# Optimization experiments

Measured on AMD Instinct MI355X. Metric: run time of the kernel, lower is better.

Reference implementation:

```python
import jax, jax.numpy as jnp
import numpy as np

NUM_CODES = 512
DIM = 64
B, M = 32, 64


def setup_inputs() -> dict:
    key = jax.random.key(0)
    k1, k2 = jax.random.split(key)
    inputs = jax.random.normal(k1, (B, M, M, DIM), dtype=jnp.float32)
    # keras 'uniform' initializer is U(-0.05, 0.05)
    embeddings = jax.random.uniform(k2, (NUM_CODES, DIM), dtype=jnp.float32,
                                    minval=-0.05, maxval=0.05)
    return {"inputs": inputs, "embeddings": embeddings}


def reference(inputs, embeddings):
    l2_inputs = jnp.sum(inputs * inputs, axis=-1, keepdims=True)      # [B,M,M,1]
    l2_embeddings = jnp.sum(embeddings * embeddings, axis=-1)          # [K]
    dot = jnp.einsum('bhwd,kd->bhwk', inputs, embeddings)              # [B,M,M,K]
    distance = l2_inputs + l2_embeddings - 2.0 * dot                   # [B,M,M,K]
    codes = jnp.argmin(distance, axis=-1).astype(jnp.int32)            # [B,M,M]
    code_vecs = embeddings[codes]                                      # [B,M,M,D]
    return codes, code_vecs
```

## Files before the change

kernel.cpp:

```cpp
#include <hip/hip_runtime.h>

#define NUM_CODES 512
#define DIM 64
#define NPIX (32 * 64 * 64)
#define CT (NUM_CODES / 16)
#define BLK 256
#define NGRP 4
#define PPB 256

typedef __attribute__((ext_vector_type(8))) short bf16x8;
typedef __attribute__((ext_vector_type(4))) float f32x4;

__device__ __forceinline__ unsigned short f2bf(float f) {
    unsigned u = __float_as_uint(f);
    return (unsigned short)((u + 0x7fffu + ((u >> 16) & 1u)) >> 16);
}
__device__ __forceinline__ float bf2f(unsigned short h) {
    return __uint_as_float(((unsigned)h) << 16);
}

__global__ __launch_bounds__(256) void prep_kernel(
    const float* __restrict__ emb, unsigned short* __restrict__ AH,
    unsigned short* __restrict__ ALO, float* __restrict__ l2e,
    float* __restrict__ l2eh) {
    const int t = blockIdx.x * 256 + threadIdx.x;
    const int e0 = t * 4;
    const int c = e0 >> 6, d0 = e0 & 63;
    const float4 v = *(const float4*)(emb + c * DIM + d0);
    float f[4] = {v.x, v.y, v.z, v.w};
    unsigned short h[4], l[4];
#pragma unroll
    for (int i = 0; i < 4; ++i) {
        h[i] = f2bf(f[i]);
        l[i] = f2bf(f[i] - bf2f(h[i]));
    }
    const int ct = c >> 4, mr = c & 15, s = d0 >> 5, q = (d0 & 31) >> 3,
              j0 = d0 & 7;
    const int base = ((ct * 2 + s) * 64 + (q * 16 + mr)) * 8 + j0;
    *(ushort4*)(AH + base) = make_ushort4(h[0], h[1], h[2], h[3]);
    *(ushort4*)(ALO + base) = make_ushort4(l[0], l[1], l[2], l[3]);

    if (t < NUM_CODES) {
        const float* e = emb + t * DIM;
        float r[8];
#pragma unroll
        for (int j = 0; j < 8; ++j) {
            float w = e[j];
            r[j] = w * w;
        }
#pragma unroll
        for (int i = 8; i < DIM; i += 8)
#pragma unroll
            for (int j = 0; j < 8; ++j) {
                float w = e[i + j];
                r[j] += w * w;
            }
        float sv =
            ((r[0] + r[1]) + (r[2] + r[3])) + ((r[4] + r[5]) + (r[6] + r[7]));
        l2e[t] = sv;
        l2eh[t] = 0.5f * sv;
    }
}

__global__ __launch_bounds__(BLK, 2) void vq_main(
    const float* __restrict__ x_in, const unsigned short* __restrict__ AH,
    const unsigned short* __restrict__ ALO, const float* __restrict__ l2e,
    const float* __restrict__ l2eh, const float* __restrict__ emb,
    float* __restrict__ codes_out, float* __restrict__ vecs_out) {
    __shared__ float s_l2eh[NUM_CODES];
    __shared__ float s_l2ex[NUM_CODES];
    __shared__ int s_top[PPB][2];
    __shared__ int s_code[PPB];

    const int tid = threadIdx.x, lane = tid & 63, wave = tid >> 6;
    s_l2eh[tid] = l2eh[tid];
    s_l2eh[tid + 256] = l2eh[tid + 256];
    s_l2ex[tid] = l2e[tid];
    s_l2ex[tid + 256] = l2e[tid + 256];
    __syncthreads();

    const int p = lane & 15, q = lane >> 4;
    const int pw = blockIdx.x * PPB + wave * (16 * NGRP);

    bf16x8 bh0[NGRP], bl0[NGRP], bh1[NGRP], bl1[NGRP];
#pragma unroll
    for (int g = 0; g < NGRP; ++g) {
        const float* xb = x_in + (size_t)(pw + g * 16 + p) * DIM + q * 8;
        float4 u0 = *(const float4*)(xb);
        float4 u1 = *(const float4*)(xb + 4);
        float4 u2 = *(const float4*)(xb + 32);
        float4 u3 = *(const float4*)(xb + 36);
        float f0[8] = {u0.x, u0.y, u0.z, u0.w, u1.x, u1.y, u1.z, u1.w};
        float f1[8] = {u2.x, u2.y, u2.z, u2.w, u3.x, u3.y, u3.z, u3.w};
#pragma unroll
        for (int j = 0; j < 8; ++j) {
            unsigned short hh = f2bf(f0[j]);
            bh0[g][j] = (short)hh;
            bl0[g][j] = (short)f2bf(f0[j] - bf2f(hh));
            unsigned short h2 = f2bf(f1[j]);
            bh1[g][j] = (short)h2;
            bl1[g][j] = (short)f2bf(f1[j] - bf2f(h2));
        }
    }

    const int rowbase = q * 4;
    float d1[NGRP], d2[NGRP];
    int k1[NGRP], k2[NGRP];
#pragma unroll
    for (int g = 0; g < NGRP; ++g) {
        d1[g] = 3.4e38f;
        d2[g] = 3.4e38f;
        k1[g] = 0;
        k2[g] = 0;
    }

    const unsigned short* pAH = AH + lane * 8;
    const unsigned short* pAL = ALO + lane * 8;
    for (int ct = 0; ct < CT; ++ct) {
        const bf16x8 a0h = *(const bf16x8*)(pAH + ct * 1024);
        const bf16x8 a0l = *(const bf16x8*)(pAL + ct * 1024);
        const bf16x8 a1h = *(const bf16x8*)(pAH + ct * 1024 + 512);
        const bf16x8 a1l = *(const bf16x8*)(pAL + ct * 1024 + 512);
        const int kb = ct * 16 + rowbase;
        float l2v[4];
#pragma unroll
        for (int r = 0; r < 4; ++r) l2v[r] = s_l2eh[kb + r];

#pragma unroll
        for (int g = 0; g < NGRP; ++g) {
            f32x4 acc = {0.f, 0.f, 0.f, 0.f};
            acc = __builtin_amdgcn_mfma_f32_16x16x32_bf16(a0h, bh0[g], acc, 0, 0, 0);
            acc = __builtin_amdgcn_mfma_f32_16x16x32_bf16(a1h, bh1[g], acc, 0, 0, 0);
            acc = __builtin_amdgcn_mfma_f32_16x16x32_bf16(a0l, bh0[g], acc, 0, 0, 0);
            acc = __builtin_amdgcn_mfma_f32_16x16x32_bf16(a1l, bh1[g], acc, 0, 0, 0);
            acc = __builtin_amdgcn_mfma_f32_16x16x32_bf16(a0h, bl0[g], acc, 0, 0, 0);
            acc = __builtin_amdgcn_mfma_f32_16x16x32_bf16(a1h, bl1[g], acc, 0, 0, 0);

#pragma unroll
            for (int r = 0; r < 4; ++r) {
                const float d = l2v[r] - acc[r];
                const int kk = kb + r;
                const bool c = d < d1[g], c2 = d < d2[g];
                const float nd2 = c2 ? d : d2[g];
                const int nk2 = c2 ? kk : k2[g];
                d2[g] = c ? d1[g] : nd2;
                k2[g] = c ? k1[g] : nk2;
                k1[g] = c ? kk : k1[g];
                d1[g] = c ? d : d1[g];
            }
        }
    }

#pragma unroll
    for (int g = 0; g < NGRP; ++g) {
        float a1 = d1[g], a2 = d2[g];
        int b1 = k1[g], b2 = k2[g];
#pragma unroll
        for (int off = 16; off <= 32; off <<= 1) {
            const float od1 = __shfl_xor(a1, off);
            const int ok1 = __shfl_xor(b1, off);
            const float od2 = __shfl_xor(a2, off);
            const int ok2 = __shfl_xor(b2, off);
            const bool c = od1 < a1;
            const float w1 = c ? od1 : a1;
            const int wk1 = c ? ok1 : b1;
            const float l1 = c ? a1 : od1;
            const int lk1 = c ? b1 : ok1;
            const bool cm = od2 < a2;
            const float m2 = cm ? od2 : a2;
            const int mk2 = cm ? ok2 : b2;
            const bool c3 = m2 < l1;
            a2 = c3 ? m2 : l1;
            b2 = c3 ? mk2 : lk1;
            a1 = w1;
            b1 = wk1;
        }
        if (lane < 16) {
            s_top[wave * (16 * NGRP) + g * 16 + lane][0] = b1;
            s_top[wave * (16 * NGRP) + g * 16 + lane][1] = b2;
        }
    }
    __syncthreads();

    {
        const int pix = blockIdx.x * PPB + tid;
        int ka = s_top[tid][0], kb2 = s_top[tid][1];
        if (kb2 < ka) {
            const int tt = ka;
            ka = kb2;
            kb2 = tt;
        }
        const float* xr = x_in + (size_t)pix * DIM;
        float x[DIM];
#pragma unroll
        for (int jj = 0; jj < 16; ++jj) {
            const float4 v = *(const float4*)(xr + jj * 4);
            x[4 * jj + 0] = v.x;
            x[4 * jj + 1] = v.y;
            x[4 * jj + 2] = v.z;
            x[4 * jj + 3] = v.w;
        }
        float r[8];
#pragma unroll
        for (int j = 0; j < 8; ++j) r[j] = x[j] * x[j];
#pragma unroll
        for (int i = 8; i < DIM; i += 8)
#pragma unroll
            for (int j = 0; j < 8; ++j) r[j] += x[i + j] * x[i + j];
        const float l2x =
            ((r[0] + r[1]) + (r[2] + r[3])) + ((r[4] + r[5]) + (r[6] + r[7]));

        const float* ea = emb + (size_t)ka * DIM;
        float acca = 0.f;
#pragma unroll
        for (int d = 0; d < DIM; ++d) acca = __builtin_fmaf(x[d], ea[d], acca);
        const float da = (l2x + s_l2ex[ka]) - 2.0f * acca;

        const float* eb = emb + (size_t)kb2 * DIM;
        float accb = 0.f;
#pragma unroll
        for (int d = 0; d < DIM; ++d) accb = __builtin_fmaf(x[d], eb[d], accb);
        const float db = (l2x + s_l2ex[kb2]) - 2.0f * accb;

        const int sel = (db < da) ? kb2 : ka;
        s_code[tid] = sel;
        codes_out[pix] = (float)sel;
    }
    __syncthreads();

    const float4* emb4 = (const float4*)emb;
    float4* vout4 = (float4*)(vecs_out + (size_t)blockIdx.x * PPB * DIM);
#pragma unroll
    for (int it = 0; it < (PPB * DIM / 4) / BLK; ++it) {
        const int fidx = tid + it * BLK;
        const int pp = fidx >> 4, dd = fidx & 15;
        vout4[fidx] = emb4[(size_t)s_code[pp] * (DIM / 4) + dd];
    }
}

extern "C" void kernel_launch(void* const* d_in, const int* in_sizes, int n_in,
                              void* d_out, int out_size, void* d_ws,
                              size_t ws_size, hipStream_t stream) {
    const float* x_in = (const float*)d_in[0];
    const float* emb = (const float*)d_in[1];

    unsigned short* AH = (unsigned short*)d_ws;
    unsigned short* ALO = AH + NUM_CODES * DIM;
    float* l2e = (float*)(ALO + NUM_CODES * DIM);
    float* l2eh = l2e + NUM_CODES;

    float* codes_out = (float*)d_out;
    float* vecs_out = (float*)d_out + NPIX;

    hipLaunchKernelGGL(prep_kernel, dim3(32), dim3(256), 0, stream, emb, AH,
                       ALO, l2e, l2eh);
    hipLaunchKernelGGL(vq_main, dim3(NPIX / PPB), dim3(BLK), 0, stream, x_in,
                       AH, ALO, l2e, l2eh, emb, codes_out, vecs_out);
}
```

Measured before the change: 127.9 us.

## Split codebook search across two wave halves and merge top-2 candidates

Doubles the block to 512 threads. Each half of the waves scans half of the codebook tiles for the same 256 pixels, then the two per-half top-2 lists are merged in shared memory. The exact fp32 refinement is also split: each of two threads computes the distance for one candidate, and the results are combined through shared memory. The aim is more waves per pixel tile, hiding MFMA and load latency and halving the serial loop length. The cost is extra shared memory, extra barriers, and a tighter register budget under launch_bounds(512,2), which could cause spilling.

```diff
diff --git a/kernel.cpp b/kernel.cpp
--- a/kernel.cpp
+++ b/kernel.cpp
@@ -3,10 +3,10 @@
 #define NUM_CODES 512
 #define DIM 64
 #define NPIX (32 * 64 * 64)
-#define CT (NUM_CODES / 16)
-#define BLK 256
+#define BLK 512
 #define NGRP 4
 #define PPB 256
+#define CTH 16
 
 typedef __attribute__((ext_vector_type(8))) short bf16x8;
 typedef __attribute__((ext_vector_type(4))) float f32x4;
@@ -69,18 +69,21 @@
     float* __restrict__ codes_out, float* __restrict__ vecs_out) {
     __shared__ float s_l2eh[NUM_CODES];
     __shared__ float s_l2ex[NUM_CODES];
-    __shared__ int s_top[PPB][2];
+    __shared__ float s_d1h[2][PPB];
+    __shared__ float s_d2h[2][PPB];
+    __shared__ int s_k1h[2][PPB];
+    __shared__ int s_k2h[2][PPB];
+    __shared__ float s_dbuf[PPB];
     __shared__ int s_code[PPB];
 
     const int tid = threadIdx.x, lane = tid & 63, wave = tid >> 6;
+    const int wgrp = wave & 3, whalf = wave >> 2;
     s_l2eh[tid] = l2eh[tid];
-    s_l2eh[tid + 256] = l2eh[tid + 256];
     s_l2ex[tid] = l2e[tid];
-    s_l2ex[tid + 256] = l2e[tid + 256];
     __syncthreads();
 
     const int p = lane & 15, q = lane >> 4;
-    const int pw = blockIdx.x * PPB + wave * (16 * NGRP);
+    const int pw = blockIdx.x * PPB + wgrp * (16 * NGRP);
 
     bf16x8 bh0[NGRP], bl0[NGRP], bh1[NGRP], bl1[NGRP];
 #pragma unroll
@@ -116,12 +119,13 @@
 
     const unsigned short* pAH = AH + lane * 8;
     const unsigned short* pAL = ALO + lane * 8;
-    for (int ct = 0; ct < CT; ++ct) {
-        const bf16x8 a0h = *(const bf16x8*)(pAH + ct * 1024);
-        const bf16x8 a0l = *(const bf16x8*)(pAL + ct * 1024);
-        const bf16x8 a1h = *(const bf16x8*)(pAH + ct * 1024 + 512);
-        const bf16x8 a1l = *(const bf16x8*)(pAL + ct * 1024 + 512);
-        const int kb = ct * 16 + rowbase;
+    for (int ct = 0; ct < CTH; ++ct) {
+        const int gt = whalf * CTH + ct;
+        const bf16x8 a0h = *(const bf16x8*)(pAH + gt * 1024);
+        const bf16x8 a0l = *(const bf16x8*)(pAL + gt * 1024);
+        const bf16x8 a1h = *(const bf16x8*)(pAH + gt * 1024 + 512);
+        const bf16x8 a1l = *(const bf16x8*)(pAL + gt * 1024 + 512);
+        const int kb = gt * 16 + rowbase;
         float l2v[4];
 #pragma unroll
         for (int r = 0; r < 4; ++r) l2v[r] = s_l2eh[kb + r];
@@ -176,20 +180,41 @@
             b1 = wk1;
         }
         if (lane < 16) {
-            s_top[wave * (16 * NGRP) + g * 16 + lane][0] = b1;
-            s_top[wave * (16 * NGRP) + g * 16 + lane][1] = b2;
+            const int pb = wgrp * 64 + g * 16 + lane;
+            s_d1h[whalf][pb] = a1;
+            s_k1h[whalf][pb] = b1;
+            s_d2h[whalf][pb] = a2;
+            s_k2h[whalf][pb] = b2;
         }
     }
     __syncthreads();
 
+    const int pp = tid & 255;
+    const int pix = blockIdx.x * PPB + pp;
+    int ka, kb;
     {
-        const int pix = blockIdx.x * PPB + tid;
-        int ka = s_top[tid][0], kb2 = s_top[tid][1];
-        if (kb2 < ka) {
-            const int tt = ka;
-            ka = kb2;
-            kb2 = tt;
-        }
+        const float d1a = s_d1h[0][pp], d1b = s_d1h[1][pp];
+        const float d2a = s_d2h[0][pp], d2b = s_d2h[1][pp];
+        const int k1a = s_k1h[0][pp], k1b = s_k1h[1][pp];
+        const int k2a = s_k2h[0][pp], k2b = s_k2h[1][pp];
+        const bool bw = d1b < d1a;
+        const int bestk = bw ? k1b : k1a;
+        const float w2 = bw ? d2b : d2a;
+        const int wk2 = bw ? k2b : k2a;
+        const float lo1 = bw ? d1a : d1b;
+        const int lok1 = bw ? k1a : k1b;
+        const bool c2 = (w2 < lo1) || (w2 == lo1 && wk2 < lok1);
+        const int k2nd = c2 ? wk2 : lok1;
+        ka = bestk;
+        kb = k2nd;
+        if (kb < ka) {
+            const int t = ka;
+            ka = kb;
+            kb = t;
+        }
+    }
+    {
+        const int myk = (tid < 256) ? ka : kb;
         const float* xr = x_in + (size_t)pix * DIM;
         float x[DIM];
 #pragma unroll
@@ -210,21 +235,20 @@
         const float l2x =
             ((r[0] + r[1]) + (r[2] + r[3])) + ((r[4] + r[5]) + (r[6] + r[7]));
 
-        const float* ea = emb + (size_t)ka * DIM;
-        float acca = 0.f;
-#pragma unroll
-        for (int d = 0; d < DIM; ++d) acca = __builtin_fmaf(x[d], ea[d], acca);
-        const float da = (l2x + s_l2ex[ka]) - 2.0f * acca;
-
-        const float* eb = emb + (size_t)kb2 * DIM;
-        float accb = 0.f;
-#pragma unroll
-        for (int d = 0; d < DIM; ++d) accb = __builtin_fmaf(x[d], eb[d], accb);
-        const float db = (l2x + s_l2ex[kb2]) - 2.0f * accb;
-
-        const int sel = (db < da) ? kb2 : ka;
-        s_code[tid] = sel;
-        codes_out[pix] = (float)sel;
+        const float* er = emb + (size_t)myk * DIM;
+        float acc = 0.f;
+#pragma unroll
+        for (int d = 0; d < DIM; ++d) acc = __builtin_fmaf(x[d], er[d], acc);
+        const float dist = (l2x + s_l2ex[myk]) - 2.0f * acc;
+        if (tid >= 256) s_dbuf[pp] = dist;
+        __syncthreads();
+        if (tid < 256) {
+            const float da = dist;
+            const float db = s_dbuf[pp];
+            const int sel = (db < da) ? kb : ka;
+            s_code[pp] = sel;
+            codes_out[pix] = (float)sel;
+        }
     }
     __syncthreads();
 
@@ -233,8 +257,8 @@
 #pragma unroll
     for (int it = 0; it < (PPB * DIM / 4) / BLK; ++it) {
         const int fidx = tid + it * BLK;
-        const int pp = fidx >> 4, dd = fidx & 15;
-        vout4[fidx] = emb4[(size_t)s_code[pp] * (DIM / 4) + dd];
+        const int ppx = fidx >> 4, dd = fidx & 15;
+        vout4[fidx] = emb4[(size_t)s_code[ppx] * (DIM / 4) + dd];
     }
 }
 
```

Result: slower. 137.5 us (+7.6%).

## Halve pixels per block, prefetch codebook tiles, split refinement across threads

Applied to the files above, without the earlier changes.

Cuts pixels per block from 256 to 128 (two MFMA groups per wave instead of four) and raises the launch-bounds occupancy hint from 2 to 4 blocks, aiming for more waves in flight and more blocks in the grid. The codebook A-fragments for the next tile are loaded before the current tile's MFMAs to hide global-load latency. The exact fp32 re-check of the two candidates is now split so each of two threads per pixel computes one distance, exchanged through shared memory with an extra barrier. The trade-off is that each pixel's 64-float input row is loaded by two threads, and the codebook is streamed by twice as many blocks.

```diff
diff --git a/kernel.cpp b/kernel.cpp
--- a/kernel.cpp
+++ b/kernel.cpp
@@ -5,8 +5,8 @@
 #define NPIX (32 * 64 * 64)
 #define CT (NUM_CODES / 16)
 #define BLK 256
-#define NGRP 4
-#define PPB 256
+#define NGRP 2
+#define PPB 128
 
 typedef __attribute__((ext_vector_type(8))) short bf16x8;
 typedef __attribute__((ext_vector_type(4))) float f32x4;
@@ -62,7 +62,7 @@
     }
 }
 
-__global__ __launch_bounds__(BLK, 2) void vq_main(
+__global__ __launch_bounds__(BLK, 4) void vq_main(
     const float* __restrict__ x_in, const unsigned short* __restrict__ AH,
     const unsigned short* __restrict__ ALO, const float* __restrict__ l2e,
     const float* __restrict__ l2eh, const float* __restrict__ emb,
@@ -70,6 +70,7 @@
     __shared__ float s_l2eh[NUM_CODES];
     __shared__ float s_l2ex[NUM_CODES];
     __shared__ int s_top[PPB][2];
+    __shared__ float s_dbuf[PPB];
     __shared__ int s_code[PPB];
 
     const int tid = threadIdx.x, lane = tid & 63, wave = tid >> 6;
@@ -116,11 +117,19 @@
 
     const unsigned short* pAH = AH + lane * 8;
     const unsigned short* pAL = ALO + lane * 8;
+
+    bf16x8 a0h = *(const bf16x8*)(pAH);
+    bf16x8 a0l = *(const bf16x8*)(pAL);
+    bf16x8 a1h = *(const bf16x8*)(pAH + 512);
+    bf16x8 a1l = *(const bf16x8*)(pAL + 512);
+
     for (int ct = 0; ct < CT; ++ct) {
-        const bf16x8 a0h = *(const bf16x8*)(pAH + ct * 1024);
-        const bf16x8 a0l = *(const bf16x8*)(pAL + ct * 1024);
-        const bf16x8 a1h = *(const bf16x8*)(pAH + ct * 1024 + 512);
-        const bf16x8 a1l = *(const bf16x8*)(pAL + ct * 1024 + 512);
+        const int nt = (ct + 1) & (CT - 1);
+        const bf16x8 n0h = *(const bf16x8*)(pAH + nt * 1024);
+        const bf16x8 n0l = *(const bf16x8*)(pAL + nt * 1024);
+        const bf16x8 n1h = *(const bf16x8*)(pAH + nt * 1024 + 512);
+        const bf16x8 n1l = *(const bf16x8*)(pAL + nt * 1024 + 512);
+
         const int kb = ct * 16 + rowbase;
         float l2v[4];
 #pragma unroll
@@ -149,6 +158,10 @@
                 d1[g] = c ? d : d1[g];
             }
         }
+        a0h = n0h;
+        a0l = n0l;
+        a1h = n1h;
+        a1l = n1l;
     }
 
 #pragma unroll
@@ -176,20 +189,25 @@
             b1 = wk1;
         }
         if (lane < 16) {
-            s_top[wave * (16 * NGRP) + g * 16 + lane][0] = b1;
-            s_top[wave * (16 * NGRP) + g * 16 + lane][1] = b2;
+            const int pb = wave * (16 * NGRP) + g * 16 + lane;
+            s_top[pb][0] = b1;
+            s_top[pb][1] = b2;
         }
     }
     __syncthreads();
 
     {
-        const int pix = blockIdx.x * PPB + tid;
-        int ka = s_top[tid][0], kb2 = s_top[tid][1];
+        const int pp = tid & (PPB - 1);
+        const int cand = tid >> 7;
+        const int pix = blockIdx.x * PPB + pp;
+        int ka = s_top[pp][0], kb2 = s_top[pp][1];
         if (kb2 < ka) {
-            const int tt = ka;
+            const int t = ka;
             ka = kb2;
-            kb2 = tt;
-        }
+            kb2 = t;
+        }
+        const int myk = cand ? kb2 : ka;
+
         const float* xr = x_in + (size_t)pix * DIM;
         float x[DIM];
 #pragma unroll
@@ -210,21 +228,21 @@
         const float l2x =
             ((r[0] + r[1]) + (r[2] + r[3])) + ((r[4] + r[5]) + (r[6] + r[7]));
 
-        const float* ea = emb + (size_t)ka * DIM;
-        float acca = 0.f;
-#pragma unroll
-        for (int d = 0; d < DIM; ++d) acca = __builtin_fmaf(x[d], ea[d], acca);
-        const float da = (l2x + s_l2ex[ka]) - 2.0f * acca;
-
-        const float* eb = emb + (size_t)kb2 * DIM;
-        float accb = 0.f;
-#pragma unroll
-        for (int d = 0; d < DIM; ++d) accb = __builtin_fmaf(x[d], eb[d], accb);
-        const float db = (l2x + s_l2ex[kb2]) - 2.0f * accb;
-
-        const int sel = (db < da) ? kb2 : ka;
-        s_code[tid] = sel;
-        codes_out[pix] = (float)sel;
+        const float* er = emb + (size_t)myk * DIM;
+        float acc = 0.f;
+#pragma unroll
+        for (int d = 0; d < DIM; ++d) acc = __builtin_fmaf(x[d], er[d], acc);
+        const float dist = (l2x + s_l2ex[myk]) - 2.0f * acc;
+
+        if (cand) s_dbuf[pp] = dist;
+        __syncthreads();
+        if (!cand) {
+            const float da = dist;
+            const float db = s_dbuf[pp];
+            const int sel = (db < da) ? kb2 : ka;
+            s_code[pp] = sel;
+            codes_out[pix] = (float)sel;
+        }
     }
     __syncthreads();
 
```

Result: no change. 129.1 us (+1.0%).
